# Optimization experiments

Hardware: AMD Instinct MI355X
Metric: run time of the kernel (lower is better)

The kernel has to match this reference:

```python
import jax
import jax.numpy as jnp
import numpy as np

B = 128          # graphs per batch
N = 1024         # nodes per graph
EG = 16384       # edges per graph (shared structure, repeated edge_weight)
F_IN = 64        # num_features
HID = 128        # hid_channels (ChebConv out)
K = 3            # Chebyshev order
C1 = HID // 2    # conv1d out channels
C2 = C1 // 2     # fc1 out
N_CLASSES = 4
POWER_ITERS = 50


def setup_inputs() -> dict:
    key = jax.random.key(0)
    ks = jax.random.split(key, 8)
    x = jax.random.normal(ks[0], (B * N, F_IN), dtype=jnp.float32)
    edge_index = jax.random.randint(ks[1], (2, EG), 0, N, dtype=jnp.int32)
    edge_weight = jax.random.uniform(ks[2], (EG,), dtype=jnp.float32)
    cheb_W = 0.05 * jax.random.normal(ks[3], (K, F_IN, HID), dtype=jnp.float32)
    cheb_b = jnp.zeros((HID,), jnp.float32)
    conv1d_W = 0.05 * jax.random.normal(ks[4], (C1, HID), dtype=jnp.float32)
    conv1d_b = jnp.zeros((C1,), jnp.float32)
    fc1_W = 0.01 * jax.random.normal(ks[5], (C2, C1 * N), dtype=jnp.float32)
    fc1_b = jnp.zeros((C2,), jnp.float32)
    fc2_W = 0.05 * jax.random.normal(ks[6], (N_CLASSES, C2), dtype=jnp.float32)
    fc2_b = jnp.zeros((N_CLASSES,), jnp.float32)
    return {"x": x, "edge_index": edge_index, "edge_weight": edge_weight,
            "cheb_W": cheb_W, "cheb_b": cheb_b,
            "conv1d_W": conv1d_W, "conv1d_b": conv1d_b,
            "fc1_W": fc1_W, "fc1_b": fc1_b, "fc2_W": fc2_W, "fc2_b": fc2_b}


def _lambda_max(edge_index, w):
    # LaplacianLambdaMax(normalization=None): largest eig of L = D - W, on raw
    # (un-relu'd) edge_attr, computed as a non-differentiable data transform.
    src, dst = edge_index[0], edge_index[1]
    deg = jax.ops.segment_sum(w, src, num_segments=N)

    def mv(v):  # L @ v
        return deg * v - jax.ops.segment_sum(w * v[src], dst, num_segments=N)

    def body(i, v):
        u = mv(v)
        return u / (jnp.linalg.norm(u) + 1e-12)

    v0 = jnp.ones((N,), jnp.float32) / np.float32(np.sqrt(N))
    v = jax.lax.fori_loop(0, POWER_ITERS, body, v0)
    return jax.lax.stop_gradient(jnp.vdot(v, mv(v)))


def _forward(x, edge_index, edge_weight, cheb_W, cheb_b, conv1d_W, conv1d_b,
             fc1_W, fc1_b, fc2_W, fc2_b):
    lmax = _lambda_max(edge_index, edge_weight)

    # Tile the shared per-graph edge structure over the batch (block-diagonal).
    offs = jnp.arange(B, dtype=jnp.int32) * N                  # [B]
    src = (edge_index[0][None, :] + offs[:, None]).reshape(-1)  # [B*EG]
    dst = (edge_index[1][None, :] + offs[:, None]).reshape(-1)  # [B*EG]
    w = jax.nn.relu(jnp.tile(edge_weight, B))                   # relu(edge_attr)

    BN = B * N
    deg = jax.ops.segment_sum(w, src, num_segments=BN)          # [BN]
    scale = 2.0 / lmax

    def lhat_mv(X):  # (2 L / lmax - I) @ X ; L = D - W
        agg = jax.ops.segment_sum(w[:, None] * X[src], dst, num_segments=BN)
        return scale * (deg[:, None] * X - agg) - X

    # Chebyshev recursion, K = 3
    tx0 = x                               # [BN, F_IN]
    tx1 = lhat_mv(tx0)
    tx2 = 2.0 * lhat_mv(tx1) - tx0
    h = tx0 @ cheb_W[0] + tx1 @ cheb_W[1] + tx2 @ cheb_W[2] + cheb_b  # [BN, HID]

    # 1x1 conv1d over the node axis + relu
    hb = h.reshape(B, N, HID)
    c = jax.nn.relu(jnp.einsum('bnh,ch->bcn', hb, conv1d_W)
                    + conv1d_b[None, :, None])                  # [B, C1, N]
    flat = c.reshape(B, C1 * N)

    z = flat @ fc1_W.T + fc1_b
    z = z @ fc2_W.T + fc2_b                                     # [B, N_CLASSES]
    return jax.nn.softmax(z, axis=1)


def reference(x, edge_index, edge_weight, cheb_W, cheb_b, conv1d_W, conv1d_b,
              fc1_W, fc1_b, fc2_W, fc2_b):
    return _forward(x, edge_index, edge_weight, cheb_W, cheb_b, conv1d_W,
                    conv1d_b, fc1_W, fc1_b, fc2_W, fc2_b)
```

## Files before the change

kernel.cpp:

```cpp
#include <hip/hip_runtime.h>
#include <math.h>

#define BATCH 128
#define NNODE 1024
#define EG 16384
#define F_IN 64
#define HID 128
#define C1 64
#define C2 32
#define NCLS 4
#define POWER_ITERS 50
#define BN (BATCH * NNODE)
#define RMAX 28
#define NORM_EVERY 5

typedef float f32x4 __attribute__((ext_vector_type(4)));
typedef __bf16 bf16x8 __attribute__((ext_vector_type(8)));
typedef unsigned short u16x4 __attribute__((ext_vector_type(4)));

__device__ inline unsigned short f2bf(float f) {
    unsigned int u = __float_as_uint(f);
    u += 0x7fffu + ((u >> 16) & 1u);
    return (unsigned short)(u >> 16);
}
__device__ inline float bf2f(unsigned short h) {
    return __uint_as_float((unsigned int)h << 16);
}

__global__ __launch_bounds__(1024) void k_csr(
    const int* __restrict__ ei, const float* __restrict__ ew,
    int* __restrict__ ptr_g, float* __restrict__ dgr_g,
    float* __restrict__ dgl_g, int2* __restrict__ packed,
    int2* __restrict__ packed2)
{
    __shared__ int   cnt[NNODE];
    __shared__ float dgr[NNODE];
    __shared__ float dgl[NNODE];
    __shared__ int   s[NNODE];
    __shared__ int   base[NNODE];
    const int t = threadIdx.x;

    cnt[t] = 0; dgr[t] = 0.f; dgl[t] = 0.f;

    int es[16], ed[16];
    float w[16];
#pragma unroll
    for (int i = 0; i < 16; ++i) {
        const int e = i * 1024 + t;
        es[i] = ei[e];
        ed[i] = ei[EG + e];
        w[i]  = ew[e];
    }
    __syncthreads();
#pragma unroll
    for (int i = 0; i < 16; ++i) {
        atomicAdd(&cnt[ed[i]], 1);
        atomicAdd(&dgr[es[i]], w[i]);
        atomicAdd(&dgl[es[i]], fmaxf(w[i], 0.f));
    }
    __syncthreads();
    dgr_g[t] = dgr[t];
    dgl_g[t] = dgl[t];

    const int v = cnt[t];
    s[t] = v;
    __syncthreads();
    for (int o = 1; o < 1024; o <<= 1) {
        const int add = (t >= o) ? s[t - o] : 0;
        __syncthreads();
        s[t] += add;
        __syncthreads();
    }
    const int excl = s[t] - v;
    ptr_g[t] = excl;
    base[t]  = excl;
    if (t == 1023) ptr_g[1024] = s[1023];
    __syncthreads();

#pragma unroll
    for (int i = 0; i < 16; ++i) {
        const int p = atomicAdd(&base[ed[i]], 1);
        packed[p]  = make_int2(__float_as_int(w[i]), es[i]);
        packed2[p] = make_int2(__float_as_int(fmaxf(w[i], 0.f)), es[i] << 8);
    }
}

__global__ __launch_bounds__(256) void k_cvtw(
    const float* __restrict__ chebW, const float* __restrict__ convW,
    unsigned short* __restrict__ wcatT, unsigned short* __restrict__ cvw)
{
    const int i = blockIdx.x * 256 + threadIdx.x;
    if (i < 24576) {
        const int n = i / 192, k = i % 192;
        wcatT[i] = f2bf(chebW[k * 128 + n]);
    }
    const int j = i - 24576;
    if (j >= 0 && j < 8192) cvw[j] = f2bf(convW[j]);
}

__global__ __launch_bounds__(1024) void k_lmax(
    const int2* __restrict__ packed, const int* __restrict__ ptr,
    const float* __restrict__ deg_raw, float* __restrict__ scal)
{
    __shared__ float vA[NNODE];
    __shared__ float vB[NNODE];
    __shared__ float red[17];
    const int t = threadIdx.x;

    const int p0 = ptr[t], p1 = ptr[t + 1];
    float w[RMAX];
    int src[RMAX];
#pragma unroll
    for (int i = 0; i < RMAX; ++i) {
        if (p0 + i < p1) {
            const int2 e = packed[p0 + i];
            w[i] = __int_as_float(e.x);
            src[i] = e.y;
        } else {
            w[i] = 0.f;
            src[i] = 0;
        }
    }
    const int tp0 = p0 + RMAX;
    const float dgv = deg_raw[t];

    vA[t] = 0.03125f;
    __syncthreads();

    float* cur = vA;
    float* nxt = vB;

    for (int it = 0; it < POWER_ITERS; ++it) {
        float u = dgv * cur[t];
#pragma unroll
        for (int i = 0; i < RMAX; ++i) u -= w[i] * cur[src[i]];
        for (int p = tp0; p < p1; ++p) {
            const int2 e = packed[p];
            u -= __int_as_float(e.x) * cur[e.y];
        }
        if ((it % NORM_EVERY) == NORM_EVERY - 1) {
            float sr = u * u;
#pragma unroll
            for (int o = 32; o > 0; o >>= 1) sr += __shfl_down(sr, o, 64);
            if ((t & 63) == 0) red[t >> 6] = sr;
            __syncthreads();
            if (t < 64) {
                float xs = (t < 16) ? red[t] : 0.f;
#pragma unroll
                for (int o = 8; o > 0; o >>= 1) xs += __shfl_down(xs, o, 64);
                if (t == 0) red[16] = 1.0f / (sqrtf(xs) + 1e-12f);
            }
            __syncthreads();
            nxt[t] = u * red[16];
        } else {
            nxt[t] = u;
        }
        __syncthreads();
        float* tmp = cur; cur = nxt; nxt = tmp;
    }

    float u = dgv * cur[t];
#pragma unroll
    for (int i = 0; i < RMAX; ++i) u -= w[i] * cur[src[i]];
    for (int p = tp0; p < p1; ++p) {
        const int2 e = packed[p];
        u -= __int_as_float(e.x) * cur[e.y];
    }
    float sr = cur[t] * u;
#pragma unroll
    for (int o = 32; o > 0; o >>= 1) sr += __shfl_down(sr, o, 64);
    if ((t & 63) == 0) red[t >> 6] = sr;
    __syncthreads();
    if (t == 0) {
        float lm = 0.f;
        for (int i = 0; i < 16; ++i) lm += red[i];
        scal[0] = lm;
        scal[1] = 2.0f / lm;
    }
}

__global__ __launch_bounds__(256) void k_prop(
    const float* __restrict__ in, const float* __restrict__ base,
    const int2* __restrict__ pk2, const int* __restrict__ ptrg,
    const float* __restrict__ deg_relu, const float* __restrict__ scal,
    float* __restrict__ out32, unsigned short* __restrict__ tcat,
    int slice, int writeX, float A, float Bc)
{
    const int bid  = ((blockIdx.x & 7) << 12) + (blockIdx.x >> 3);
    const int lane = threadIdx.x & 63;
    const int gnode = __builtin_amdgcn_readfirstlane(bid * 4 + (threadIdx.x >> 6));
    const int b = gnode >> 10, d = gnode & 1023;

    const int p0 = __builtin_amdgcn_readfirstlane(ptrg[d]);
    const int p1 = __builtin_amdgcn_readfirstlane(ptrg[d + 1]);
    const char* xb = (const char*)(in + (size_t)b * (NNODE * F_IN));

    float acc = 0.f;
    int p = p0;
    for (; p + 4 <= p1; p += 4) {
        const int2 e0 = pk2[p],     e1 = pk2[p + 1];
        const int2 e2 = pk2[p + 2], e3 = pk2[p + 3];
        const float* r0 = (const float*)(xb + (unsigned)e0.y);
        const float* r1 = (const float*)(xb + (unsigned)e1.y);
        const float* r2 = (const float*)(xb + (unsigned)e2.y);
        const float* r3 = (const float*)(xb + (unsigned)e3.y);
        const float v0 = r0[lane];
        const float v1 = r1[lane];
        const float v2 = r2[lane];
        const float v3 = r3[lane];
        acc += __int_as_float(e0.x) * v0;
        acc += __int_as_float(e1.x) * v1;
        acc += __int_as_float(e2.x) * v2;
        acc += __int_as_float(e3.x) * v3;
    }
    for (; p < p1; ++p) {
        const int2 e = pk2[p];
        const float* r = (const float*)(xb + (unsigned)e.y);
        acc += __int_as_float(e.x) * r[lane];
    }

    const float scale = scal[1];
    const size_t gi = (size_t)gnode * F_IN + lane;
    const float xv = in[gi];
    const float r = scale * (deg_relu[d] * xv - acc) - xv;
    float o = A * r;
    if (Bc != 0.0f) o += Bc * base[gi];
    if (out32) out32[gi] = o;
    tcat[(size_t)gnode * 192 + slice * 64 + lane] = f2bf(o);
    if (writeX) tcat[(size_t)gnode * 192 + lane] = f2bf(xv);
}

__global__ __launch_bounds__(256) void k_cheb_mfma(
    const unsigned short* __restrict__ tcat,
    const unsigned short* __restrict__ wcatT,
    const unsigned short* __restrict__ cvw,
    const float* __restrict__ chebB, const float* __restrict__ convB,
    unsigned short* __restrict__ cout)
{
    __shared__ __align__(16) char smem[49152];
    __shared__ float cb_s[HID];
    __shared__ float cvb_s[C1];

    const int t    = threadIdx.x;
    const int lane = t & 63;
    const int wid  = t >> 6;
    const int l15  = lane & 15;
    const int l4   = lane >> 4;
    const int rbase = blockIdx.x * 128;
    const int bb = rbase >> 10;
    const int n0 = rbase & 1023;

    if (t < HID) cb_s[t] = chebB[t];
    if (t < C1)  cvb_s[t] = convB[t];

    for (int it = 0; it < 12; ++it) {
        const int gslot = it * 256 + t;
        const int n = gslot / 24, q = gslot % 24;
        const bf16x8 v = *(const bf16x8*)(wcatT + n * 192 + q * 8);
        *(bf16x8*)(smem + n * 384 + ((q ^ (n & 7)) << 4)) = v;
    }
    __syncthreads();

    const int rw = rbase + wid * 32;
    f32x4 acc[2][8];
#pragma unroll
    for (int m = 0; m < 2; ++m)
#pragma unroll
        for (int n = 0; n < 8; ++n) acc[m][n] = (f32x4)(0.f);

    const unsigned short* ta = tcat + (size_t)(rw + l15) * 192 + l4 * 8;
    bf16x8 a0 = *(const bf16x8*)(ta);
    bf16x8 a1 = *(const bf16x8*)(ta + 16 * 192);

#pragma unroll
    for (int ks = 0; ks < 6; ++ks) {
        bf16x8 na0, na1;
        if (ks < 5) {
            na0 = *(const bf16x8*)(ta + (ks + 1) * 32);
            na1 = *(const bf16x8*)(ta + 16 * 192 + (ks + 1) * 32);
        }
        const int kb = ks * 4 + l4;
#pragma unroll
        for (int nb = 0; nb < 8; ++nb) {
            const int n = nb * 16 + l15;
            const bf16x8 bv =
                *(const bf16x8*)(smem + n * 384 + ((kb ^ (n & 7)) << 4));
            acc[0][nb] = __builtin_amdgcn_mfma_f32_16x16x32_bf16(
                a0, bv, acc[0][nb], 0, 0, 0);
            acc[1][nb] = __builtin_amdgcn_mfma_f32_16x16x32_bf16(
                a1, bv, acc[1][nb], 0, 0, 0);
        }
        a0 = na0; a1 = na1;
    }
    __syncthreads();

#pragma unroll
    for (int mf = 0; mf < 2; ++mf)
#pragma unroll
        for (int nb = 0; nb < 8; ++nb) {
            const int c = nb * 16 + l15;
            const int slot = c >> 3;
            const float cb = cb_s[c];
#pragma unroll
            for (int reg = 0; reg < 4; ++reg) {
                const int node = wid * 32 + mf * 16 + l4 * 4 + reg;
                *(unsigned short*)(smem + node * 256 +
                                   ((slot ^ (node & 7)) << 4) + (c & 7) * 2) =
                    f2bf(acc[mf][nb][reg] + cb);
            }
        }
    for (int it = 0; it < 4; ++it) {
        const int gslot = it * 256 + t;
        const int c1i = gslot >> 4, q = gslot & 15;
        const bf16x8 v = *(const bf16x8*)(cvw + c1i * 128 + q * 8);
        *(bf16x8*)(smem + 32768 + c1i * 256 + ((q ^ (c1i & 7)) << 4)) = v;
    }
    __syncthreads();

    f32x4 acc2[8];
#pragma unroll
    for (int n = 0; n < 8; ++n) acc2[n] = (f32x4)(0.f);

#pragma unroll
    for (int ks = 0; ks < 4; ++ks) {
        const int kb = ks * 4 + l4;
        const int c1a = wid * 16 + l15;
        const bf16x8 av = *(const bf16x8*)(smem + 32768 + c1a * 256 +
                                           ((kb ^ (c1a & 7)) << 4));
#pragma unroll
        for (int nb = 0; nb < 8; ++nb) {
            const int node = nb * 16 + l15;
            const bf16x8 bv =
                *(const bf16x8*)(smem + node * 256 + ((kb ^ (node & 7)) << 4));
            acc2[nb] = __builtin_amdgcn_mfma_f32_16x16x32_bf16(
                av, bv, acc2[nb], 0, 0, 0);
        }
    }

#pragma unroll
    for (int nb = 0; nb < 8; ++nb) {
        const int ng = n0 + nb * 16 + l15;
#pragma unroll
        for (int reg = 0; reg < 4; ++reg) {
            const int c1i = wid * 16 + l4 * 4 + reg;
            cout[(size_t)bb * (C1 * NNODE) + (size_t)c1i * NNODE + ng] =
                f2bf(fmaxf(acc2[nb][reg] + cvb_s[c1i], 0.f));
        }
    }
}

__global__ __launch_bounds__(256) void k_fc1(
    const unsigned short* __restrict__ cf, const float* __restrict__ W,
    float* __restrict__ part)
{
    __shared__ float Wt[256 * 33];
    const int t = threadIdx.x;
    const int g = blockIdx.x;
    const int k0 = g * 256;

    for (int i = t; i < 8192; i += 256) {
        const int j = i >> 8, k = i & 255;
        Wt[k * 33 + j] = W[(size_t)j * (C1 * NNODE) + k0 + k];
    }
    __syncthreads();

    const int j = t & 31, bg = t >> 5;
    float acc[16];
#pragma unroll
    for (int i = 0; i < 16; ++i) acc[i] = 0.f;

    const unsigned short* cb = cf + (size_t)(bg * 16) * (C1 * NNODE) + k0;
    for (int k4 = 0; k4 < 64; ++k4) {
        const int kb = k4 * 4;
        const float w0 = Wt[(kb + 0) * 33 + j];
        const float w1 = Wt[(kb + 1) * 33 + j];
        const float w2 = Wt[(kb + 2) * 33 + j];
        const float w3 = Wt[(kb + 3) * 33 + j];
#pragma unroll
        for (int i = 0; i < 16; ++i) {
            const u16x4 cv = *(const u16x4*)&cb[(size_t)i * (C1 * NNODE) + kb];
            acc[i] += bf2f(cv[0]) * w0 + bf2f(cv[1]) * w1 +
                      bf2f(cv[2]) * w2 + bf2f(cv[3]) * w3;
        }
    }
#pragma unroll
    for (int i = 0; i < 16; ++i)
        part[(size_t)g * 4096 + (size_t)(bg * 16 + i) * 32 + j] = acc[i];
}

__global__ __launch_bounds__(256) void k_red(
    const float* __restrict__ part, float* __restrict__ z)
{
    const int o = blockIdx.x * 256 + threadIdx.x;
    float s = 0.f;
    for (int g = 0; g < 256; ++g) s += part[(size_t)g * 4096 + o];
    z[o] = s;
}

__global__ __launch_bounds__(128) void k_head(
    const float* __restrict__ z, const float* __restrict__ b1,
    const float* __restrict__ W2, const float* __restrict__ b2,
    float* __restrict__ outp)
{
    const int b = threadIdx.x;
    float a[32];
#pragma unroll
    for (int j = 0; j < 32; ++j) a[j] = z[b * 32 + j] + b1[j];
    float l[4];
#pragma unroll
    for (int c = 0; c < 4; ++c) {
        float s = b2[c];
#pragma unroll
        for (int j = 0; j < 32; ++j) s += W2[c * 32 + j] * a[j];
        l[c] = s;
    }
    const float m = fmaxf(fmaxf(l[0], l[1]), fmaxf(l[2], l[3]));
    const float e0 = expf(l[0] - m), e1 = expf(l[1] - m);
    const float e2 = expf(l[2] - m), e3 = expf(l[3] - m);
    const float inv = 1.f / (e0 + e1 + e2 + e3);
    outp[b * 4 + 0] = e0 * inv;
    outp[b * 4 + 1] = e1 * inv;
    outp[b * 4 + 2] = e2 * inv;
    outp[b * 4 + 3] = e3 * inv;
}

extern "C" void kernel_launch(void* const* d_in, const int* in_sizes, int n_in,
                              void* d_out, int out_size, void* d_ws, size_t ws_size,
                              hipStream_t stream)
{
    const float* x     = (const float*)d_in[0];
    const int*   ei    = (const int*)d_in[1];
    const float* ew    = (const float*)d_in[2];
    const float* chebW = (const float*)d_in[3];
    const float* chebB = (const float*)d_in[4];
    const float* convW = (const float*)d_in[5];
    const float* convB = (const float*)d_in[6];
    const float* fc1W  = (const float*)d_in[7];
    const float* fc1B  = (const float*)d_in[8];
    const float* fc2W  = (const float*)d_in[9];
    const float* fc2B  = (const float*)d_in[10];
    float* out = (float*)d_out;

    char* ws = (char*)d_ws;
    float* scal = (float*)(ws + 0);
    char*  partb = ws + 8192;
    int*   ptr  = (int*)(partb + 8192);
    float* dgr  = (float*)(partb + 16384);
    float* dgl  = (float*)(partb + 20480);
    int2*  pk   = (int2*)(partb + 24576);
    unsigned short* wcatT = (unsigned short*)(partb + 262144);
    unsigned short* cvwB  = (unsigned short*)(partb + 327680);
    int2*  pk2  = (int2*)(partb + 458752);
    float* part = (float*)partb;
    float* z    = (float*)(ws + 8192 + 4194304);
    float* tx1  = (float*)(ws + 8192 + 4194304 + 65536);
    unsigned short* tcat = (unsigned short*)((char*)tx1 + 33554432);
    unsigned short* cbuf = (unsigned short*)((char*)tcat + 50331648);

    k_csr <<<dim3(1),   dim3(1024), 0, stream>>>(ei, ew, ptr, dgr, dgl, pk, pk2);
    k_cvtw<<<dim3(128), dim3(256),  0, stream>>>(chebW, convW, wcatT, cvwB);

    k_lmax<<<dim3(1), dim3(1024), 0, stream>>>(pk, ptr, dgr, scal);

    k_prop<<<dim3(BN / 4), dim3(256), 0, stream>>>(
        x, x, pk2, ptr, dgl, scal, tx1, tcat, 1, 1, 1.f, 0.f);
    k_prop<<<dim3(BN / 4), dim3(256), 0, stream>>>(
        tx1, x, pk2, ptr, dgl, scal, (float*)nullptr, tcat, 2, 0, 2.f, -1.f);

    k_cheb_mfma<<<dim3(BN / 128), dim3(256), 0, stream>>>(
        tcat, wcatT, cvwB, chebB, convB, cbuf);

    k_fc1<<<dim3(256), dim3(256), 0, stream>>>(cbuf, fc1W, part);
    k_red<<<dim3(16), dim3(256), 0, stream>>>(part, z);
    k_head<<<dim3(1), dim3(128), 0, stream>>>(z, fc1B, fc2W, fc2B, out);
}
```

Baseline: 304.6 us.

## Fold Chebyshev scaling into weights and overlap power iteration with propagation

The Chebyshev recursion is rewritten algebraically. The propagation kernels now compute the raw Laplacian products L·x and L·(L·x), and the lmax-dependent scale and the T0/T1/T2 combination are folded into the bf16 weight matrix, which is built after lmax is known. Because propagation no longer depends on lmax, the serial single-block power iteration is split in half and placed in block 0 of each fused propagation launch, so it overlaps with the gather work. This removes the standalone serial lmax kernel from the critical path. In exchange, the power-iteration state must round-trip through global memory, and the changed numerics of L² in bf16 with scaling applied later could shift accuracy.

Result: faster. 268.0 us (-12.0%).

```diff
diff --git a/kernel.cpp b/kernel.cpp
--- a/kernel.cpp
+++ b/kernel.cpp
@@ -87,108 +87,123 @@
 
 __global__ __launch_bounds__(256) void k_cvtw(
     const float* __restrict__ chebW, const float* __restrict__ convW,
+    const float* __restrict__ scal,
     unsigned short* __restrict__ wcatT, unsigned short* __restrict__ cvw)
 {
     const int i = blockIdx.x * 256 + threadIdx.x;
+    const float s = scal[1];
     if (i < 24576) {
-        const int n = i / 192, k = i % 192;
-        wcatT[i] = f2bf(chebW[k * 128 + n]);
+        const int n = i / 192, kk = i % 192;
+        const int k = kk & 63;
+        const float w0 = chebW[k * 128 + n];
+        const float w1 = chebW[8192 + k * 128 + n];
+        const float w2 = chebW[16384 + k * 128 + n];
+        float val;
+        if (kk < 64)       val = w0 - w1 + w2;
+        else if (kk < 128) val = s * (w1 - 4.f * w2);
+        else               val = 2.f * s * s * w2;
+        wcatT[i] = f2bf(val);
     }
     const int j = i - 24576;
     if (j >= 0 && j < 8192) cvw[j] = f2bf(convW[j]);
 }
 
-__global__ __launch_bounds__(1024) void k_lmax(
-    const int2* __restrict__ packed, const int* __restrict__ ptr,
-    const float* __restrict__ deg_raw, float* __restrict__ scal)
+__global__ __launch_bounds__(1024) void k_fused(
+    const float* __restrict__ in,
+    const int2* __restrict__ pk_raw, const int2* __restrict__ pk2,
+    const int* __restrict__ ptrg,
+    const float* __restrict__ dgr, const float* __restrict__ dgl,
+    float* __restrict__ vstate, float* __restrict__ scal,
+    float* __restrict__ out32, unsigned short* __restrict__ tcat,
+    int slice, int writeX, int it0, int it1, int finalize)
 {
     __shared__ float vA[NNODE];
     __shared__ float vB[NNODE];
     __shared__ float red[17];
     const int t = threadIdx.x;
 
-    const int p0 = ptr[t], p1 = ptr[t + 1];
-    float w[RMAX];
-    int src[RMAX];
-#pragma unroll
-    for (int i = 0; i < RMAX; ++i) {
-        if (p0 + i < p1) {
-            const int2 e = packed[p0 + i];
-            w[i] = __int_as_float(e.x);
-            src[i] = e.y;
-        } else {
-            w[i] = 0.f;
-            src[i] = 0;
-        }
-    }
-    const int tp0 = p0 + RMAX;
-    const float dgv = deg_raw[t];
-
-    vA[t] = 0.03125f;
-    __syncthreads();
-
-    float* cur = vA;
-    float* nxt = vB;
-
-    for (int it = 0; it < POWER_ITERS; ++it) {
+    if (blockIdx.x == 0) {
+        const int p0 = ptrg[t], p1 = ptrg[t + 1];
+        float w[RMAX];
+        int src[RMAX];
+#pragma unroll
+        for (int i = 0; i < RMAX; ++i) {
+            if (p0 + i < p1) {
+                const int2 e = pk_raw[p0 + i];
+                w[i] = __int_as_float(e.x);
+                src[i] = e.y;
+            } else {
+                w[i] = 0.f;
+                src[i] = 0;
+            }
+        }
+        const int tp0 = p0 + RMAX;
+        const float dgv = dgr[t];
+
+        vA[t] = (it0 == 0) ? 0.03125f : vstate[t];
+        __syncthreads();
+
+        float* cur = vA;
+        float* nxt = vB;
+
+        for (int it = it0; it < it1; ++it) {
+            float u = dgv * cur[t];
+#pragma unroll
+            for (int i = 0; i < RMAX; ++i) u -= w[i] * cur[src[i]];
+            for (int p = tp0; p < p1; ++p) {
+                const int2 e = pk_raw[p];
+                u -= __int_as_float(e.x) * cur[e.y];
+            }
+            if ((it % NORM_EVERY) == NORM_EVERY - 1) {
+                float sr = u * u;
+#pragma unroll
+                for (int o = 32; o > 0; o >>= 1) sr += __shfl_down(sr, o, 64);
+                if ((t & 63) == 0) red[t >> 6] = sr;
+                __syncthreads();
+                if (t < 64) {
+                    float xs = (t < 16) ? red[t] : 0.f;
+#pragma unroll
+                    for (int o = 8; o > 0; o >>= 1) xs += __shfl_down(xs, o, 64);
+                    if (t == 0) red[16] = 1.0f / (sqrtf(xs) + 1e-12f);
+                }
+                __syncthreads();
+                nxt[t] = u * red[16];
+            } else {
+                nxt[t] = u;
+            }
+            __syncthreads();
+            float* tmp = cur; cur = nxt; nxt = tmp;
+        }
+
+        if (!finalize) {
+            vstate[t] = cur[t];
+            return;
+        }
         float u = dgv * cur[t];
 #pragma unroll
         for (int i = 0; i < RMAX; ++i) u -= w[i] * cur[src[i]];
         for (int p = tp0; p < p1; ++p) {
-            const int2 e = packed[p];
+            const int2 e = pk_raw[p];
             u -= __int_as_float(e.x) * cur[e.y];
         }
-        if ((it % NORM_EVERY) == NORM_EVERY - 1) {
-            float sr = u * u;
-#pragma unroll
-            for (int o = 32; o > 0; o >>= 1) sr += __shfl_down(sr, o, 64);
-            if ((t & 63) == 0) red[t >> 6] = sr;
-            __syncthreads();
-            if (t < 64) {
-                float xs = (t < 16) ? red[t] : 0.f;
-#pragma unroll
-                for (int o = 8; o > 0; o >>= 1) xs += __shfl_down(xs, o, 64);
-                if (t == 0) red[16] = 1.0f / (sqrtf(xs) + 1e-12f);
-            }
-            __syncthreads();
-            nxt[t] = u * red[16];
-        } else {
-            nxt[t] = u;
-        }
+        float sr = cur[t] * u;
+#pragma unroll
+        for (int o = 32; o > 0; o >>= 1) sr += __shfl_down(sr, o, 64);
+        if ((t & 63) == 0) red[t >> 6] = sr;
         __syncthreads();
-        float* tmp = cur; cur = nxt; nxt = tmp;
-    }
-
-    float u = dgv * cur[t];
-#pragma unroll
-    for (int i = 0; i < RMAX; ++i) u -= w[i] * cur[src[i]];
-    for (int p = tp0; p < p1; ++p) {
-        const int2 e = packed[p];
-        u -= __int_as_float(e.x) * cur[e.y];
-    }
-    float sr = cur[t] * u;
-#pragma unroll
-    for (int o = 32; o > 0; o >>= 1) sr += __shfl_down(sr, o, 64);
-    if ((t & 63) == 0) red[t >> 6] = sr;
-    __syncthreads();
-    if (t == 0) {
-        float lm = 0.f;
-        for (int i = 0; i < 16; ++i) lm += red[i];
-        scal[0] = lm;
-        scal[1] = 2.0f / lm;
-    }
-}
-
-__global__ __launch_bounds__(256) void k_prop(
-    const float* __restrict__ in, const float* __restrict__ base,
-    const int2* __restrict__ pk2, const int* __restrict__ ptrg,
-    const float* __restrict__ deg_relu, const float* __restrict__ scal,
-    float* __restrict__ out32, unsigned short* __restrict__ tcat,
-    int slice, int writeX, float A, float Bc)
-{
-    const int bid  = ((blockIdx.x & 7) << 12) + (blockIdx.x >> 3);
+        if (t == 0) {
+            float lm = 0.f;
+            for (int i = 0; i < 16; ++i) lm += red[i];
+            scal[0] = lm;
+            scal[1] = 2.0f / lm;
+        }
+        return;
+    }
+
+    const int b1   = blockIdx.x - 1;
+    const int bid  = ((b1 & 7) << 10) + (b1 >> 3);
     const int lane = threadIdx.x & 63;
-    const int gnode = __builtin_amdgcn_readfirstlane(bid * 4 + (threadIdx.x >> 6));
+    const int gnode = __builtin_amdgcn_readfirstlane(bid * 16 + (threadIdx.x >> 6));
     const int b = gnode >> 10, d = gnode & 1023;
 
     const int p0 = __builtin_amdgcn_readfirstlane(ptrg[d]);
@@ -200,14 +215,10 @@
     for (; p + 4 <= p1; p += 4) {
         const int2 e0 = pk2[p],     e1 = pk2[p + 1];
         const int2 e2 = pk2[p + 2], e3 = pk2[p + 3];
-        const float* r0 = (const float*)(xb + (unsigned)e0.y);
-        const float* r1 = (const float*)(xb + (unsigned)e1.y);
-        const float* r2 = (const float*)(xb + (unsigned)e2.y);
-        const float* r3 = (const float*)(xb + (unsigned)e3.y);
-        const float v0 = r0[lane];
-        const float v1 = r1[lane];
-        const float v2 = r2[lane];
-        const float v3 = r3[lane];
+        const float v0 = ((const float*)(xb + (unsigned)e0.y))[lane];
+        const float v1 = ((const float*)(xb + (unsigned)e1.y))[lane];
+        const float v2 = ((const float*)(xb + (unsigned)e2.y))[lane];
+        const float v3 = ((const float*)(xb + (unsigned)e3.y))[lane];
         acc += __int_as_float(e0.x) * v0;
         acc += __int_as_float(e1.x) * v1;
         acc += __int_as_float(e2.x) * v2;
@@ -215,16 +226,12 @@
     }
     for (; p < p1; ++p) {
         const int2 e = pk2[p];
-        const float* r = (const float*)(xb + (unsigned)e.y);
-        acc += __int_as_float(e.x) * r[lane];
-    }
-
-    const float scale = scal[1];
+        acc += __int_as_float(e.x) * ((const float*)(xb + (unsigned)e.y))[lane];
+    }
+
     const size_t gi = (size_t)gnode * F_IN + lane;
     const float xv = in[gi];
-    const float r = scale * (deg_relu[d] * xv - acc) - xv;
-    float o = A * r;
-    if (Bc != 0.0f) o += Bc * base[gi];
+    const float o = dgl[d] * xv - acc;
     if (out32) out32[gi] = o;
     tcat[(size_t)gnode * 192 + slice * 64 + lane] = f2bf(o);
     if (writeX) tcat[(size_t)gnode * 192 + lane] = f2bf(xv);
@@ -442,7 +449,8 @@
     float* out = (float*)d_out;
 
     char* ws = (char*)d_ws;
-    float* scal = (float*)(ws + 0);
+    float* scal   = (float*)(ws + 0);
+    float* vstate = (float*)(ws + 4096);
     char*  partb = ws + 8192;
     int*   ptr  = (int*)(partb + 8192);
     float* dgr  = (float*)(partb + 16384);
@@ -453,19 +461,20 @@
     int2*  pk2  = (int2*)(partb + 458752);
     float* part = (float*)partb;
     float* z    = (float*)(ws + 8192 + 4194304);
-    float* tx1  = (float*)(ws + 8192 + 4194304 + 65536);
-    unsigned short* tcat = (unsigned short*)((char*)tx1 + 33554432);
+    float* y1   = (float*)(ws + 8192 + 4194304 + 65536);
+    unsigned short* tcat = (unsigned short*)((char*)y1 + 33554432);
     unsigned short* cbuf = (unsigned short*)((char*)tcat + 50331648);
 
-    k_csr <<<dim3(1),   dim3(1024), 0, stream>>>(ei, ew, ptr, dgr, dgl, pk, pk2);
-    k_cvtw<<<dim3(128), dim3(256),  0, stream>>>(chebW, convW, wcatT, cvwB);
-
-    k_lmax<<<dim3(1), dim3(1024), 0, stream>>>(pk, ptr, dgr, scal);
-
-    k_prop<<<dim3(BN / 4), dim3(256), 0, stream>>>(
-        x, x, pk2, ptr, dgl, scal, tx1, tcat, 1, 1, 1.f, 0.f);
-    k_prop<<<dim3(BN / 4), dim3(256), 0, stream>>>(
-        tx1, x, pk2, ptr, dgl, scal, (float*)nullptr, tcat, 2, 0, 2.f, -1.f);
+    k_csr <<<dim3(1), dim3(1024), 0, stream>>>(ei, ew, ptr, dgr, dgl, pk, pk2);
+
+    k_fused<<<dim3(BN / 16 + 1), dim3(1024), 0, stream>>>(
+        x, pk, pk2, ptr, dgr, dgl, vstate, scal,
+        y1, tcat, 1, 1, 0, 25, 0);
+    k_fused<<<dim3(BN / 16 + 1), dim3(1024), 0, stream>>>(
+        y1, pk, pk2, ptr, dgr, dgl, vstate, scal,
+        (float*)nullptr, tcat, 2, 0, 25, 50, 1);
+
+    k_cvtw<<<dim3(128), dim3(256), 0, stream>>>(chebW, convW, scal, wcatT, cvwB);
 
     k_cheb_mfma<<<dim3(BN / 128), dim3(256), 0, stream>>>(
         tcat, wcatT, cvwB, chebB, convB, cbuf);
```
